# Optimization experiments

Measured on AMD Instinct MI355X. Metric: run time of the kernel, lower is better.

## Reference

```python
import jax, jax.numpy as jnp
import numpy as np


def _cell_centered_coords(H, W):
    # cell-centered unit grid: coordinate k -> (k + 0.5) / n, meshgrid over (h1, w1, h2, w2)
    h = (jnp.arange(H, dtype=jnp.float32) + 0.5) / H
    w = (jnp.arange(W, dtype=jnp.float32) + 0.5) / W
    g = jnp.meshgrid(h, w, h, w, indexing='ij')
    return jnp.stack(g, axis=-1)  # (H, W, H, W, 4)


def setup_inputs() -> dict:
    key = jax.random.key(0)
    ks = jax.random.split(key, 6)
    B, I, O, H, W, HID = 8, 16, 16, 28, 28, 64
    s1 = 1.0 / np.sqrt(4.0)
    s2 = 1.0 / np.sqrt(HID)
    return {
        'v': jax.random.normal(ks[0], (B, I, H, W), dtype=jnp.float32),
        'W1': jax.random.uniform(ks[1], (4, HID), jnp.float32, -s1, s1),
        'b1': jax.random.uniform(ks[2], (HID,), jnp.float32, -s1, s1),
        'W2': jax.random.uniform(ks[3], (HID, O * I), jnp.float32, -s2, s2),
        'b2': jax.random.uniform(ks[4], (O * I,), jnp.float32, -s2, s2),
        'bias': jax.random.uniform(ks[5], (O, 1, 1), jnp.float32, -1.0 / np.sqrt(I), 1.0 / np.sqrt(I)),
    }


def reference(v, W1, b1, W2, b2, bias):
    H, W = v.shape[-2], v.shape[-1]
    I = v.shape[-3]
    O = W2.shape[-1] // I
    coords = _cell_centered_coords(H, W)                      # (H,W,H,W,4)
    hidden = jax.nn.gelu(coords @ W1 + b1, approximate=False)  # (H,W,H,W,64)
    kernel = (hidden @ W2 + b2).reshape(H, W, H, W, O, I)      # (h1,w1,h2,w2,O,I)
    # midpoint-rule quadrature weights on the unit square: 1/(H*W) per cell
    quad = 1.0 / (H * W)
    # einsum 'h1 w1 h2 w2 o i, n i h1 w2 -> n o h2 w2' (w1 summed out of kernel alone)
    out = jnp.einsum('pqrsoi,nips->nors', kernel, quad * v)
    return out + bias
```

## Files before the change

### kernel.cpp

```cpp
#include <hip/hip_runtime.h>

#define Hn 28
#define PQ 784
#define NI 128

typedef __attribute__((ext_vector_type(8))) short short8v;
typedef __attribute__((ext_vector_type(4))) short short4v;
typedef __attribute__((ext_vector_type(4))) float float4v;

__device__ __forceinline__ short f2bf(float x) {
    union { float f; unsigned u; } a; a.f = x;
    unsigned r = a.u + 0x7FFF + ((a.u >> 16) & 1);
    return (short)(r >> 16);
}

__global__ __launch_bounds__(256) void prep_kernel(
    const float* __restrict__ v, const float* __restrict__ W2,
    short* __restrict__ vTb, short* __restrict__ W2b, float* __restrict__ Vsum)
{
    const int b = blockIdx.x;
    const int t = threadIdx.x;
    if (b == NI) {
        for (int e = t; e < 8192; e += 256) {
            const float2 f = ((const float2*)W2)[e];
            short2 h; h.x = f2bf(f.x); h.y = f2bf(f.y);
            ((short2*)W2b)[e] = h;
        }
        return;
    }
    __shared__ float sT[Hn * 29];
    const int ni = b;
    #pragma unroll
    for (int k = 0; k < 4; ++k) {
        const int e = t + 256 * k;
        if (e < PQ) {
            const int p = e / Hn;
            const int s = e - p * Hn;
            sT[s * 29 + p] = v[ni * PQ + e];
        }
    }
    __syncthreads();
    #pragma unroll
    for (int k = 0; k < 2; ++k) {
        const int idx = t + 256 * k;
        if (idx < Hn * 16) {
            const int s = idx >> 4;
            const int e2 = idx & 15;
            const int p0 = 2 * e2;
            short2 h;
            h.x = (p0     < Hn) ? f2bf(sT[s * 29 + p0])     : (short)0;
            h.y = (p0 + 1 < Hn) ? f2bf(sT[s * 29 + p0 + 1]) : (short)0;
            *(short2*)(vTb + s * (NI * 32) + ni * 32 + p0) = h;
        }
    }
    if (t < Hn) {
        const int s = t;
        float acc = 0.0f;
        #pragma unroll
        for (int p = 0; p < Hn; ++p) acc += sT[s * 29 + p];
        Vsum[s * NI + ni] = acc;
    }
}

__global__ __launch_bounds__(256, 4) void fused_kernel(
    const short* __restrict__ vTb, const short* __restrict__ W2b,
    const float* __restrict__ Vsum,
    const float* __restrict__ W1, const float* __restrict__ b1,
    const float* __restrict__ b2, const float* __restrict__ bias,
    float* __restrict__ out)
{
    __shared__ short sV[NI * 40];
    __shared__ short sHt[64 * 40];
    __shared__ short sTa[8 * 1032];
    __shared__ float sRed[4 * 256];
    __shared__ float sVs[NI];

    const int t = threadIdx.x;
    const int rs = blockIdx.x;
    const int r = rs / Hn;
    const int s = rs - r * Hn;

    {
        const short* src = vTb + s * (NI * 32);
        #pragma unroll
        for (int j = 0; j < 2; ++j) {
            const int idx = t + 256 * j;
            const int ni = idx >> 2;
            const int ko = (idx & 3) * 8;
            *(short8v*)&sV[ni * 40 + ko] = *(const short8v*)(src + ni * 32 + ko);
        }
    }
    if (t < NI) sVs[t] = Vsum[s * NI + t];

    {
        const int c = t & 63;
        const int pg = t >> 6;
        const float w0 = W1[c];
        const float Wc = W1[64 + c];
        const float w2 = W1[128 + c];
        const float w3 = W1[192 + c];
        const float inv = 1.0f / 28.0f;
        const float base = ((r + 0.5f) * inv) * w2 + ((s + 0.5f) * inv) * w3
                         + b1[c] + 0.5f * Wc;
        const float w0i = inv * w0;
        const float W2c = Wc * Wc;
        const float c2 = 1.1651786f * W2c;
        const float c4 = 0.0145213f * (W2c * W2c);
        #pragma unroll
        for (int pi = 0; pi < 7; ++pi) {
            const int p = pg * 7 + pi;
            const float m  = fmaf((float)p + 0.5f, w0i, base);
            const float m2 = m * m;
            const float E  = __builtin_amdgcn_exp2f(m2 * -0.72134752f);
            const float az = fabsf(m) * 0.70710678f;
            const float tt = __builtin_amdgcn_rcpf(fmaf(0.3275911f, az, 1.0f));
            float poly = fmaf(tt, 1.061405429f, -1.453152027f);
            poly = fmaf(tt, poly, 1.421413741f);
            poly = fmaf(tt, poly, -0.284496736f);
            poly = fmaf(tt, poly, 0.254829592f);
            poly = poly * tt;
            float erfv = fmaf(-poly, E, 1.0f);
            erfv = (m < 0.0f) ? -erfv : erfv;
            const float g   = 0.5f * m * (1.0f + erfv);
            const float phi = 0.39894228f * E;
            const float p4  = fmaf(-m2, m2, fmaf(7.0f, m2, -4.0f));
            const float corr = phi * fmaf(c4, p4, c2 * (2.0f - m2));
            sHt[c * 40 + p] = f2bf(fmaf(28.0f, g, corr));
        }
        if (pg == 3) *(uint2*)&sHt[c * 40 + 28] = make_uint2(0u, 0u);
    }
    __syncthreads();

    const int w  = t >> 6;
    const int l  = t & 63;
    const int lm = l & 15;
    const int q  = l >> 4;
    const int k0 = q * 8;

    {
        short8v aF[2], bF[4];
        aF[0] = *(const short8v*)&sV[(32 * w + lm) * 40 + k0];
        aF[1] = *(const short8v*)&sV[(32 * w + 16 + lm) * 40 + k0];
        #pragma unroll
        for (int nt = 0; nt < 4; ++nt)
            bF[nt] = *(const short8v*)&sHt[(16 * nt + lm) * 40 + k0];

        float4v accD[2][4];
        #pragma unroll
        for (int mt = 0; mt < 2; ++mt)
            #pragma unroll
            for (int nt = 0; nt < 4; ++nt)
                accD[mt][nt] = __builtin_amdgcn_mfma_f32_16x16x32_bf16(
                    aF[mt], bF[nt], (float4v)(0.0f), 0, 0, 0);

        #pragma unroll
        for (int mt = 0; mt < 2; ++mt) {
            const int n8 = 2 * w + mt;
            #pragma unroll
            for (int nt = 0; nt < 4; ++nt) {
                const int c = 16 * nt + lm;
                short4v pk;
                pk[0] = f2bf(accD[mt][nt][0]);
                pk[1] = f2bf(accD[mt][nt][1]);
                pk[2] = f2bf(accD[mt][nt][2]);
                pk[3] = f2bf(accD[mt][nt][3]);
                *(short4v*)&sTa[n8 * 1032 + c * 16 + 4 * q] = pk;
            }
        }
    }
    __syncthreads();

    float4v accO = (float4v)(0.0f);
    #pragma unroll
    for (int st = 0; st < 8; ++st) {
        const int kb = w * 256 + st * 32 + k0;
        const short8v a = *(const short8v*)&sTa[(lm & 7) * 1032 + kb];
        const int c  = kb >> 4;
        const int i0 = kb & 15;
        const short8v bfr = *(const short8v*)&W2b[c * 256 + lm * 16 + i0];
        accO = __builtin_amdgcn_mfma_f32_16x16x32_bf16(a, bfr, accO, 0, 0, 0);
    }
    #pragma unroll
    for (int reg = 0; reg < 4; ++reg) {
        const int m = q * 4 + reg;
        sRed[w * 256 + m * 16 + lm] = accO[reg];
    }
    __syncthreads();

    if (t < NI) {
        const int n8 = t >> 4;
        const int o  = t & 15;
        const int e  = n8 * 16 + o;
        const float tot = sRed[e] + sRed[256 + e] + sRed[512 + e] + sRed[768 + e];
        float bsum = 0.0f;
        #pragma unroll
        for (int i = 0; i < 16; ++i)
            bsum = fmaf(b2[o * 16 + i], sVs[n8 * 16 + i], bsum);
        out[(n8 * 16 + o) * PQ + rs] = (tot + 28.0f * bsum) * (1.0f / 784.0f) + bias[o];
    }
}

extern "C" void kernel_launch(void* const* d_in, const int* in_sizes, int n_in,
                              void* d_out, int out_size, void* d_ws, size_t ws_size,
                              hipStream_t stream) {
    const float* v    = (const float*)d_in[0];
    const float* W1   = (const float*)d_in[1];
    const float* b1   = (const float*)d_in[2];
    const float* W2   = (const float*)d_in[3];
    const float* b2   = (const float*)d_in[4];
    const float* bias = (const float*)d_in[5];
    float* out = (float*)d_out;

    char* ws = (char*)d_ws;
    short* vTb  = (short*)(ws);
    short* W2b  = (short*)(ws + 229376);
    float* Vsum = (float*)(ws + 262144);

    prep_kernel<<<NI + 1, 256, 0, stream>>>(v, W2, vTb, W2b, Vsum);
    fused_kernel<<<PQ, 256, 0, stream>>>(vTb, W2b, Vsum, W1, b1, b2, bias, out);
}
```

Baseline: 72.61 us.

## Merge prep and main kernels into one cooperative launch with grid sync

Combines the bf16 conversion/transpose prep kernel and the fused compute kernel into a single cooperative kernel. The first 129 blocks do the prep work, then every block waits on a grid-wide barrier before running the main computation. The shared memory buffers are carved out of one byte array so the prep transpose can reuse it. The goal is to remove the second kernel launch and the gap between launches. In exchange it adds a grid barrier, and all 784 blocks must be co-resident for the cooperative launch to succeed.

```diff
diff --git a/kernel.cpp b/kernel.cpp
--- a/kernel.cpp
+++ b/kernel.cpp
@@ -1,4 +1,7 @@
 #include <hip/hip_runtime.h>
+#include <hip/hip_cooperative_groups.h>
+
+namespace cg = cooperative_groups;
 
 #define Hn 28
 #define PQ 784
@@ -14,69 +17,67 @@
     return (short)(r >> 16);
 }
 
-__global__ __launch_bounds__(256) void prep_kernel(
-    const float* __restrict__ v, const float* __restrict__ W2,
-    short* __restrict__ vTb, short* __restrict__ W2b, float* __restrict__ Vsum)
+__global__ __launch_bounds__(256, 4) void mono_kernel(
+    const float* __restrict__ v, const float* __restrict__ W1,
+    const float* __restrict__ b1, const float* __restrict__ W2,
+    const float* __restrict__ b2, const float* __restrict__ bias,
+    float* __restrict__ out, short* __restrict__ vTb,
+    short* __restrict__ W2b, float* __restrict__ Vsum)
 {
+    __shared__ __align__(16) char smem[36480];
+    short* sV  = (short*)smem;
+    short* sHt = (short*)(smem + 10240);
+    short* sTa = (short*)(smem + 15360);
+    float* sRed = (float*)(smem + 31872);
+    float* sVs  = (float*)(smem + 35968);
+
+    const int t = threadIdx.x;
     const int b = blockIdx.x;
-    const int t = threadIdx.x;
-    if (b == NI) {
+
+    if (b < NI) {
+        float* sT = (float*)smem;
+        const int ni = b;
+        #pragma unroll
+        for (int k = 0; k < 4; ++k) {
+            const int e = t + 256 * k;
+            if (e < PQ) {
+                const int p = e / Hn;
+                const int s = e - p * Hn;
+                sT[s * 29 + p] = v[ni * PQ + e];
+            }
+        }
+        __syncthreads();
+        #pragma unroll
+        for (int k = 0; k < 2; ++k) {
+            const int idx = t + 256 * k;
+            if (idx < Hn * 16) {
+                const int s = idx >> 4;
+                const int e2 = idx & 15;
+                const int p0 = 2 * e2;
+                short2 h;
+                h.x = (p0     < Hn) ? f2bf(sT[s * 29 + p0])     : (short)0;
+                h.y = (p0 + 1 < Hn) ? f2bf(sT[s * 29 + p0 + 1]) : (short)0;
+                *(short2*)(vTb + s * (NI * 32) + ni * 32 + p0) = h;
+            }
+        }
+        if (t < Hn) {
+            const int s = t;
+            float acc = 0.0f;
+            #pragma unroll
+            for (int p = 0; p < Hn; ++p) acc += sT[s * 29 + p];
+            Vsum[s * NI + ni] = acc;
+        }
+    } else if (b == NI) {
         for (int e = t; e < 8192; e += 256) {
             const float2 f = ((const float2*)W2)[e];
             short2 h; h.x = f2bf(f.x); h.y = f2bf(f.y);
             ((short2*)W2b)[e] = h;
         }
-        return;
-    }
-    __shared__ float sT[Hn * 29];
-    const int ni = b;
-    #pragma unroll
-    for (int k = 0; k < 4; ++k) {
-        const int e = t + 256 * k;
-        if (e < PQ) {
-            const int p = e / Hn;
-            const int s = e - p * Hn;
-            sT[s * 29 + p] = v[ni * PQ + e];
-        }
-    }
-    __syncthreads();
-    #pragma unroll
-    for (int k = 0; k < 2; ++k) {
-        const int idx = t + 256 * k;
-        if (idx < Hn * 16) {
-            const int s = idx >> 4;
-            const int e2 = idx & 15;
-            const int p0 = 2 * e2;
-            short2 h;
-            h.x = (p0     < Hn) ? f2bf(sT[s * 29 + p0])     : (short)0;
-            h.y = (p0 + 1 < Hn) ? f2bf(sT[s * 29 + p0 + 1]) : (short)0;
-            *(short2*)(vTb + s * (NI * 32) + ni * 32 + p0) = h;
-        }
-    }
-    if (t < Hn) {
-        const int s = t;
-        float acc = 0.0f;
-        #pragma unroll
-        for (int p = 0; p < Hn; ++p) acc += sT[s * 29 + p];
-        Vsum[s * NI + ni] = acc;
-    }
-}
-
-__global__ __launch_bounds__(256, 4) void fused_kernel(
-    const short* __restrict__ vTb, const short* __restrict__ W2b,
-    const float* __restrict__ Vsum,
-    const float* __restrict__ W1, const float* __restrict__ b1,
-    const float* __restrict__ b2, const float* __restrict__ bias,
-    float* __restrict__ out)
-{
-    __shared__ short sV[NI * 40];
-    __shared__ short sHt[64 * 40];
-    __shared__ short sTa[8 * 1032];
-    __shared__ float sRed[4 * 256];
-    __shared__ float sVs[NI];
-
-    const int t = threadIdx.x;
-    const int rs = blockIdx.x;
+    }
+
+    cg::this_grid().sync();
+
+    const int rs = b;
     const int r = rs / Hn;
     const int s = rs - r * Hn;
 
@@ -216,6 +217,8 @@
     short* W2b  = (short*)(ws + 229376);
     float* Vsum = (float*)(ws + 262144);
 
-    prep_kernel<<<NI + 1, 256, 0, stream>>>(v, W2, vTb, W2b, Vsum);
-    fused_kernel<<<PQ, 256, 0, stream>>>(vTb, W2b, Vsum, W1, b1, b2, bias, out);
+    void* args[] = { (void*)&v, (void*)&W1, (void*)&b1, (void*)&W2, (void*)&b2,
+                     (void*)&bias, (void*)&out, (void*)&vTb, (void*)&W2b, (void*)&Vsum };
+    hipLaunchCooperativeKernel((const void*)mono_kernel, dim3(PQ), dim3(256),
+                               args, 0, stream);
 }
```

Result: slower. 167.9 us (+131.2%).
